# Kernel tuning notes

Measured on AMD Instinct MI355X. Metric: run time of the kernel, lower is better.

The kernel has to match this reference:

```python
import jax, jax.numpy as jnp
import numpy as np

NEG_SLOPE = 0.2  # PyG GATConv default leaky_relu slope


def gat_conv(x, src, dst, W, att_src, att_dst, bias, num_nodes):
    """PyG-style GATConv with concat=False (mean over heads).
    x: [N, Fin], src/dst: [E] (self-loops already appended),
    W: [Fin, H*C], att_src/att_dst: [H, C], bias: [C].
    """
    H, C = att_src.shape
    h = (x @ W).reshape(num_nodes, H, C)               # [N, H, C]
    a_s = jnp.sum(h * att_src[None], axis=-1)          # [N, H]
    a_d = jnp.sum(h * att_dst[None], axis=-1)          # [N, H]
    e = jax.nn.leaky_relu(a_s[src] + a_d[dst], NEG_SLOPE)  # [E, H]
    # softmax over incoming edges per destination node
    e_max = jax.ops.segment_max(e, dst, num_segments=num_nodes)  # [N, H]
    e_exp = jnp.exp(e - e_max[dst])
    denom = jax.ops.segment_sum(e_exp, dst, num_segments=num_nodes)
    alpha = e_exp / (denom[dst] + 1e-16)               # [E, H]
    msg = h[src] * alpha[:, :, None]                   # [E, H, C]
    out = jax.ops.segment_sum(msg, dst, num_segments=num_nodes)  # [N, H, C]
    return out.mean(axis=1) + bias                     # concat=False -> head mean


def setup_inputs() -> dict:
    N, E = 100000, 1600000
    Fin, Hid, Fout, Hds = 128, 64, 32, 2
    key = jax.random.key(0)
    ks = jax.random.split(key, 12)
    glorot = lambda k, shape, fan: (jax.random.normal(k, shape, jnp.float32) / np.sqrt(fan))
    return {
        "x": jax.random.normal(ks[0], (N, Fin), jnp.float32),
        "edge_index": jax.random.randint(ks[1], (2, E), 0, N, jnp.int64 if jax.config.read("jax_enable_x64") else jnp.int32),
        "W1": glorot(ks[2], (Fin, Hds * Hid), Fin),
        "att_src1": glorot(ks[3], (Hds, Hid), Hid),
        "att_dst1": glorot(ks[4], (Hds, Hid), Hid),
        "b1": jnp.zeros((Hid,), jnp.float32),
        "W2": glorot(ks[5], (Hid, Hds * Fout), Hid),
        "att_src2": glorot(ks[6], (Hds, Fout), Fout),
        "att_dst2": glorot(ks[7], (Hds, Fout), Fout),
        "b2": jnp.zeros((Fout,), jnp.float32),
    }


def reference(x, edge_index, W1, att_src1, att_dst1, b1, W2, att_src2, att_dst2, b2):
    N = x.shape[0]
    # PyG GATConv default: add self-loops
    loops = jnp.arange(N, dtype=edge_index.dtype)
    src = jnp.concatenate([edge_index[0], loops])
    dst = jnp.concatenate([edge_index[1], loops])
    # dropout(p=0.6) is identity in eval mode
    h = gat_conv(x, src, dst, W1, att_src1, att_dst1, b1, N)
    h = jax.nn.elu(h)
    out = gat_conv(h, src, dst, W2, att_src2, att_dst2, b2, N)
    return out
```

## Files before the change

### kernel.cpp

```cpp
#include <hip/hip_runtime.h>
#include <hip/hip_bf16.h>
#include <hip/hip_fp16.h>
#include <math.h>


#define BINBITS 9
#define NBUCK 256
#define CHUNK 4096
#define SPANCAP 12288

typedef _Float16 half8 __attribute__((ext_vector_type(8)));
typedef float f32x4 __attribute__((ext_vector_type(4)));


__global__ void init_kernel(int* __restrict__ bcnt) {
    bcnt[threadIdx.x] = 0;
}

__global__ void bucket_hist_kernel(const int* __restrict__ dst, int* __restrict__ bcnt, int E) {
    __shared__ int h[NBUCK];
    int t = threadIdx.x;
    h[t] = 0;
    __syncthreads();
    for (int i = blockIdx.x * blockDim.x + t; i < E; i += gridDim.x * blockDim.x)
        atomicAdd(&h[dst[i] >> BINBITS], 1);
    __syncthreads();
    if (h[t]) atomicAdd(&bcnt[t], h[t]);
}

__global__ void bucket_scan_kernel(const int* __restrict__ bcnt, int* __restrict__ bbase,
                                   int* __restrict__ bfill) {
    __shared__ int sd[NBUCK];
    int t = threadIdx.x;
    int v = bcnt[t];
    sd[t] = v;
    __syncthreads();
    for (int o = 1; o < NBUCK; o <<= 1) {
        int x = (t >= o) ? sd[t - o] : 0;
        __syncthreads();
        sd[t] += x;
        __syncthreads();
    }
    int exc = sd[t] - v;
    bbase[t] = exc;
    bfill[t] = exc;
    if (t == NBUCK - 1) bbase[NBUCK] = sd[t];
}

__launch_bounds__(256)
__global__ void binA_kernel(const int* __restrict__ esrc, const int* __restrict__ edst,
                            int* __restrict__ bfill, unsigned* __restrict__ binned, int E) {
    __shared__ unsigned stage[CHUNK];
    __shared__ int hcnt[NBUCK], hexc[NBUCK], gb[NBUCK], hfill[NBUCK];
    const int tid = threadIdx.x;
    const int c0 = blockIdx.x * CHUNK;
    const int n = min(CHUNK, E - c0);

    hcnt[tid] = 0;
    hfill[tid] = 0;
    __syncthreads();
    for (int i = tid; i < n; i += 256) atomicAdd(&hcnt[edst[c0 + i] >> BINBITS], 1);
    __syncthreads();
    int myc = hcnt[tid];
    hexc[tid] = myc;
    __syncthreads();
    for (int o = 1; o < NBUCK; o <<= 1) {
        int x = (tid >= o) ? hexc[tid - o] : 0;
        __syncthreads();
        hexc[tid] += x;
        __syncthreads();
    }
    hexc[tid] -= myc;
    gb[tid] = myc ? atomicAdd(&bfill[tid], myc) : 0;
    __syncthreads();

    for (int i = tid; i < n; i += 256) {
        int d = edst[c0 + i], s = esrc[c0 + i];
        int b = d >> BINBITS;
        int p = hexc[b] + atomicAdd(&hfill[b], 1);
        stage[p] = ((unsigned)(d & ((1 << BINBITS) - 1)) << 17) | (unsigned)s;
    }
    __syncthreads();

    const int wid = tid >> 6, lane = tid & 63;
    for (int b = wid * 64; b < wid * 64 + 64; ++b) {
        int cnt = hcnt[b], sb = hexc[b], g = gb[b];
        for (int l = lane; l < cnt; l += 64) binned[g + l] = stage[sb + l];
    }
}

__launch_bounds__(256)
__global__ void binB_kernel(const unsigned* __restrict__ binned, const int* __restrict__ bbase,
                            int* __restrict__ rowptr, int* __restrict__ csr, int N) {
    __shared__ int cnt[512];
    __shared__ int chunk[256];
    __shared__ int excl[513];
    __shared__ int stag[SPANCAP];
    const int tid = threadIdx.x;
    const int b = blockIdx.x;
    const int node0 = b << BINBITS;
    if (node0 >= N) return;
    const int nn = min(512, N - node0);

    cnt[tid] = (tid < nn) ? 1 : 0;
    cnt[tid + 256] = (tid + 256 < nn) ? 1 : 0;
    __syncthreads();
    const int e0 = bbase[b], e1 = bbase[b + 1];
    for (int i = e0 + tid; i < e1; i += 256)
        atomicAdd(&cnt[binned[i] >> 17], 1);
    __syncthreads();

    int c0v = cnt[2 * tid], c1v = cnt[2 * tid + 1];
    chunk[tid] = c0v + c1v;
    __syncthreads();
    int v = chunk[tid];
    for (int o = 1; o < 256; o <<= 1) {
        int x = (tid >= o) ? chunk[tid - o] : 0;
        __syncthreads();
        chunk[tid] += x;
        __syncthreads();
    }
    int cpre = chunk[tid] - v;
    excl[2 * tid] = cpre;
    excl[2 * tid + 1] = cpre + c0v;
    if (tid == 255) excl[512] = cpre + c0v + c1v;
    __syncthreads();

    const int rbase = e0 + node0;
    for (int i = tid; i < nn; i += 256) rowptr[node0 + i] = rbase + excl[i];
    if (node0 + nn >= N && tid == 0) rowptr[N] = rbase + excl[512];

    cnt[tid] = 0;
    cnt[tid + 256] = 0;
    __syncthreads();
    const int span = excl[512];

    if (span <= SPANCAP) {
        for (int i = e0 + tid; i < e1; i += 256) {
            unsigned e = binned[i];
            int dloc = e >> 17, src = e & 0x1FFFF;
            int p = excl[dloc] + atomicAdd(&cnt[dloc], 1);
            stag[p] = src;
        }
        for (int i = tid; i < nn; i += 256) {
            int p = excl[i] + atomicAdd(&cnt[i], 1);
            stag[p] = node0 + i;
        }
        __syncthreads();
        for (int i = tid; i < span; i += 256) csr[rbase + i] = stag[i];
    } else {
        for (int i = e0 + tid; i < e1; i += 256) {
            unsigned e = binned[i];
            int dloc = e >> 17, src = e & 0x1FFFF;
            csr[rbase + excl[dloc] + atomicAdd(&cnt[dloc], 1)] = src;
        }
        for (int i = tid; i < nn; i += 256)
            csr[rbase + excl[i] + atomicAdd(&cnt[i], 1)] = node0 + i;
    }
}


__global__ void wcvt_kernel(const float* __restrict__ W1, _Float16* __restrict__ Wt1,
                            const float* __restrict__ W2, _Float16* __restrict__ Wt2) {
    int i = blockIdx.x * 256 + threadIdx.x;
    if (i < 128 * 128) {
        int n = i >> 7, k = i & 127;
        Wt1[i] = (_Float16)W1[k * 128 + n];
    }
    int j = i - 128 * 128;
    if (j >= 0 && j < 64 * 64) {
        int n = j >> 6, k = j & 63;
        Wt2[j] = (_Float16)W2[k * 64 + n];
    }
}


template <int FIN, int FOUT, typename XT>
__launch_bounds__(256)
__global__ void gemm_attn_mfma(const XT* __restrict__ X, const _Float16* __restrict__ Wt,
                               const float* __restrict__ atts, const float* __restrict__ attd,
                               __half* __restrict__ Hh, float* __restrict__ a_s,
                               float* __restrict__ a_d, int N) {
    constexpr int BM = 128;
    constexpr int C = FOUT / 2;
    constexpr int NT = FOUT / 16;
    constexpr int KS = FIN / 32;
    constexpr int HT = C / 16;
    __shared__ _Float16 sA[BM * FIN];
    __shared__ _Float16 sB[FOUT * FIN];

    const int tid = threadIdx.x;
    const int wv = tid >> 6, ln = tid & 63;
    const int lm = ln & 15, quad = ln >> 4;
    const int row0 = blockIdx.x * BM;

    if (sizeof(XT) == 4) {
        for (int idx = tid; idx < BM * FIN / 4; idx += 256) {
            int r = idx / (FIN / 4), c4 = idx % (FIN / 4);
            int gr = row0 + r;
            float4 v = make_float4(0.f, 0.f, 0.f, 0.f);
            if (gr < N) v = *(const float4*)&((const float*)X)[(size_t)gr * FIN + c4 * 4];
            _Float16 h4[4] = {(_Float16)v.x, (_Float16)v.y, (_Float16)v.z, (_Float16)v.w};
            *(float2*)&sA[r * FIN + c4 * 4] = *(float2*)h4;
        }
    } else {
        for (int idx = tid; idx < BM * FIN / 8; idx += 256) {
            int r = idx / (FIN / 8), c8 = idx % (FIN / 8);
            int gr = row0 + r;
            int4 v = make_int4(0, 0, 0, 0);
            if (gr < N) v = *(const int4*)&((const __half*)X)[(size_t)gr * FIN + c8 * 8];
            *(int4*)&sA[r * FIN + c8 * 8] = v;
        }
    }
    for (int idx = tid; idx < FOUT * FIN / 8; idx += 256)
        *(int4*)&sB[idx * 8] = *(const int4*)&Wt[idx * 8];
    __syncthreads();

    f32x4 acc[2][NT];
#pragma unroll
    for (int mt = 0; mt < 2; ++mt)
#pragma unroll
        for (int nt = 0; nt < NT; ++nt) acc[mt][nt] = f32x4{0.f, 0.f, 0.f, 0.f};

    const int r0 = wv * 32 + lm;
#pragma unroll
    for (int ks = 0; ks < KS; ++ks) {
        int k0 = ks * 32 + quad * 8;
        half8 a0 = *(const half8*)&sA[r0 * FIN + k0];
        half8 a1 = *(const half8*)&sA[(r0 + 16) * FIN + k0];
#pragma unroll
        for (int nt = 0; nt < NT; ++nt) {
            half8 b = *(const half8*)&sB[(nt * 16 + lm) * FIN + k0];
            acc[0][nt] = __builtin_amdgcn_mfma_f32_16x16x32_f16(a0, b, acc[0][nt], 0, 0, 0);
            acc[1][nt] = __builtin_amdgcn_mfma_f32_16x16x32_f16(a1, b, acc[1][nt], 0, 0, 0);
        }
    }

    float psum[2][4][2], pdum[2][4][2];
#pragma unroll
    for (int mt = 0; mt < 2; ++mt)
#pragma unroll
        for (int r = 0; r < 4; ++r) {
            psum[mt][r][0] = psum[mt][r][1] = 0.f;
            pdum[mt][r][0] = pdum[mt][r][1] = 0.f;
        }
#pragma unroll
    for (int nt = 0; nt < NT; ++nt) {
        float av = atts[nt * 16 + lm];
        float dv = attd[nt * 16 + lm];
        int hh = nt / HT;
#pragma unroll
        for (int mt = 0; mt < 2; ++mt)
#pragma unroll
            for (int r = 0; r < 4; ++r) {
                psum[mt][r][hh] = fmaf(acc[mt][nt][r], av, psum[mt][r][hh]);
                pdum[mt][r][hh] = fmaf(acc[mt][nt][r], dv, pdum[mt][r][hh]);
            }
    }
#pragma unroll
    for (int o = 1; o < 16; o <<= 1) {
#pragma unroll
        for (int mt = 0; mt < 2; ++mt)
#pragma unroll
            for (int r = 0; r < 4; ++r) {
                psum[mt][r][0] += __shfl_xor(psum[mt][r][0], o);
                psum[mt][r][1] += __shfl_xor(psum[mt][r][1], o);
                pdum[mt][r][0] += __shfl_xor(pdum[mt][r][0], o);
                pdum[mt][r][1] += __shfl_xor(pdum[mt][r][1], o);
            }
    }
    if (lm == 0) {
#pragma unroll
        for (int mt = 0; mt < 2; ++mt)
#pragma unroll
            for (int r = 0; r < 4; ++r) {
                int gr = row0 + wv * 32 + mt * 16 + quad * 4 + r;
                if (gr < N) {
                    *(float2*)&a_s[gr * 2] = make_float2(psum[mt][r][0], psum[mt][r][1]);
                    *(float2*)&a_d[gr * 2] = make_float2(pdum[mt][r][0], pdum[mt][r][1]);
                }
            }
    }

    __syncthreads();
    _Float16* sH = sA;
#pragma unroll
    for (int mt = 0; mt < 2; ++mt)
#pragma unroll
        for (int nt = 0; nt < NT; ++nt)
#pragma unroll
            for (int r = 0; r < 4; ++r)
                sH[(wv * 32 + mt * 16 + quad * 4 + r) * FOUT + nt * 16 + lm] =
                    (_Float16)acc[mt][nt][r];
    __syncthreads();
    for (int idx = tid; idx < BM * FOUT / 8; idx += 256) {
        int r = idx / (FOUT / 8), c8 = idx % (FOUT / 8);
        int gr = row0 + r;
        if (gr < N)
            *(int4*)&Hh[(size_t)gr * FOUT + c8 * 8] = *(const int4*)&sH[r * FOUT + c8 * 8];
    }
}


__device__ __forceinline__ float lrelu02(float x) { return x > 0.f ? x : 0.2f * x; }

__launch_bounds__(256)
__global__ void edge_w_kernel(const float* __restrict__ a_s, const float* __restrict__ a_d,
                              const int* __restrict__ rowptr, const int* __restrict__ csr,
                              float2* __restrict__ w, int N) {
    const int wid = threadIdx.x >> 6, lane = threadIdx.x & 63;
    int n = blockIdx.x * 4 + wid;
    if (n >= N) return;
    int start = rowptr[n], end = rowptr[n + 1];
    int deg = end - start;
    float2 adn = ((const float2*)a_d)[n];

    if (deg <= 64) {
        float e0 = 0.f, e1 = 0.f;
        int j = start + lane;
        if (lane < deg) {
            int s = csr[j];
            float2 asv = ((const float2*)a_s)[s];
            e0 = __expf(lrelu02(asv.x + adn.x));
            e1 = __expf(lrelu02(asv.y + adn.y));
        }
        float d0 = e0, d1 = e1;
#pragma unroll
        for (int o = 32; o > 0; o >>= 1) {
            d0 += __shfl_xor(d0, o);
            d1 += __shfl_xor(d1, o);
        }
        float i0 = 0.5f / d0, i1 = 0.5f / d1;
        if (lane < deg) w[j] = make_float2(e0 * i0, e1 * i1);
    } else {
        float d0 = 0.f, d1 = 0.f;
        for (int j = start + lane; j < end; j += 64) {
            int s = csr[j];
            float2 asv = ((const float2*)a_s)[s];
            float e0 = __expf(lrelu02(asv.x + adn.x));
            float e1 = __expf(lrelu02(asv.y + adn.y));
            d0 += e0;
            d1 += e1;
            w[j] = make_float2(e0, e1);
        }
#pragma unroll
        for (int o = 32; o > 0; o >>= 1) {
            d0 += __shfl_xor(d0, o);
            d1 += __shfl_xor(d1, o);
        }
        float i0 = 0.5f / d0, i1 = 0.5f / d1;
        for (int j = start + lane; j < end; j += 64) {
            float2 f = w[j];
            w[j] = make_float2(f.x * i0, f.y * i1);
        }
    }
}


template <int C, bool ELU, typename OT>
__launch_bounds__(256)
__global__ void aggregate_kernel(const __half* __restrict__ Hh, const float2* __restrict__ w,
                                 const int* __restrict__ rowptr, const int* __restrict__ csr,
                                 const float* __restrict__ bias, OT* __restrict__ out, int N) {
    constexpr int LPE = (C == 64) ? 16 : 8;
    constexpr int NG = 64 / LPE;
    constexpr int RI = C / 4;
    __shared__ float2 swH[4][64][2];
    const int wid = threadIdx.x >> 6;
    const int lane = threadIdx.x & 63;
    const int sub = lane & (LPE - 1);
    const int qid = lane / LPE;
    const int myH = (sub >= LPE / 2);
    int n = blockIdx.x * 4 + wid;
    if (n >= N) return;
    int start = rowptr[n], end = rowptr[n + 1];
    const int4* HI = (const int4*)Hh;

    float av[8];
#pragma unroll
    for (int j = 0; j < 8; ++j) av[j] = 0.f;

    for (int cs = start; cs < end; cs += 64) {
        int j = cs + lane;
        float2 wv = make_float2(0.f, 0.f);
        int s = 0;
        if (j < end) {
            s = csr[j];
            wv = w[j];
        }
        float fs = __int_as_float(s);
        swH[wid][lane][0] = make_float2(wv.x, fs);
        swH[wid][lane][1] = make_float2(wv.y, fs);
        int cnt = min(64, end - cs);
        int nbatch = (cnt + NG - 1) / NG;
        for (int b = 0; b < nbatch; b += 4) {
            float2 e[4];
#pragma unroll
            for (int u = 0; u < 4; ++u)
                e[u] = swH[wid][(b + u) * NG + qid][myH];
            int4 hv[4];
#pragma unroll
            for (int u = 0; u < 4; ++u)
                hv[u] = HI[(size_t)__float_as_int(e[u].y) * RI + sub];
#pragma unroll
            for (int u = 0; u < 4; ++u) {
                float ww = e[u].x;
                const __half2* h2 = (const __half2*)&hv[u];
#pragma unroll
                for (int p = 0; p < 4; ++p) {
                    float2 f = __half22float2(h2[p]);
                    av[2 * p] = fmaf(ww, f.x, av[2 * p]);
                    av[2 * p + 1] = fmaf(ww, f.y, av[2 * p + 1]);
                }
            }
        }
    }

#pragma unroll
    for (int o = LPE; o < 64; o <<= 1)
#pragma unroll
        for (int j = 0; j < 8; ++j) av[j] += __shfl_xor(av[j], o);
#pragma unroll
    for (int j = 0; j < 8; ++j) av[j] += __shfl_xor(av[j], LPE / 2);

    if (lane < LPE / 2) {
        float4 b0 = *(const float4*)(bias + sub * 8);
        float4 b1 = *(const float4*)(bias + sub * 8 + 4);
        float o0[8];
        o0[0] = av[0] + b0.x; o0[1] = av[1] + b0.y;
        o0[2] = av[2] + b0.z; o0[3] = av[3] + b0.w;
        o0[4] = av[4] + b1.x; o0[5] = av[5] + b1.y;
        o0[6] = av[6] + b1.z; o0[7] = av[7] + b1.w;
        if (ELU) {
#pragma unroll
            for (int j = 0; j < 8; ++j) o0[j] = o0[j] > 0.f ? o0[j] : expm1f(o0[j]);
        }
        if (sizeof(OT) == 2) {
            union { int4 v; __half2 h2[4]; } u;
#pragma unroll
            for (int p = 0; p < 4; ++p) u.h2[p] = __floats2half2_rn(o0[2 * p], o0[2 * p + 1]);
            *(int4*)((__half*)out + (size_t)n * C + sub * 8) = u.v;
        } else {
            *(float4*)((float*)out + (size_t)n * C + sub * 8) =
                make_float4(o0[0], o0[1], o0[2], o0[3]);
            *(float4*)((float*)out + (size_t)n * C + sub * 8 + 4) =
                make_float4(o0[4], o0[5], o0[6], o0[7]);
        }
    }
}


extern "C" void kernel_launch(void* const* d_in, const int* in_sizes, int n_in,
                              void* d_out, int out_size, void* d_ws, size_t ws_size,
                              hipStream_t stream) {
    const float* x    = (const float*)d_in[0];
    const int*   eidx = (const int*)d_in[1];
    const float* W1   = (const float*)d_in[2];
    const float* as1w = (const float*)d_in[3];
    const float* ad1w = (const float*)d_in[4];
    const float* b1   = (const float*)d_in[5];
    const float* W2   = (const float*)d_in[6];
    const float* as2w = (const float*)d_in[7];
    const float* ad2w = (const float*)d_in[8];
    const float* b2   = (const float*)d_in[9];
    float* out = (float*)d_out;

    const int N = in_sizes[0] / 128;
    const int E = in_sizes[1] / 2;
    const int NBK = (N + (1 << BINBITS) - 1) >> BINBITS;

    char* base = (char*)d_ws;
    size_t off = 0;
    auto alloc = [&](size_t bytes) {
        size_t cur = off;
        off += (bytes + 255) & ~(size_t)255;
        return (void*)(base + cur);
    };

    int* rowptr   = (int*)alloc((size_t)(N + 1) * 4);
    int* csr      = (int*)alloc((size_t)(E + N) * 4);
    int* bcnt     = (int*)alloc((size_t)NBUCK * 4);
    int* bbase    = (int*)alloc((size_t)(NBUCK + 1) * 4);
    int* bfill    = (int*)alloc((size_t)NBUCK * 4);
    unsigned* binned = (unsigned*)alloc((size_t)E * 4);
    __half* h1    = (__half*)alloc((size_t)N * 128 * 2);
    __half* x2h   = (__half*)alloc((size_t)N * 64 * 2);
    float* a_s    = (float*)alloc((size_t)N * 2 * 4);
    float* a_d    = (float*)alloc((size_t)N * 2 * 4);
    float2* wEdge = (float2*)alloc((size_t)(E + N) * 8);
    _Float16* Wt1 = (_Float16*)alloc((size_t)128 * 128 * 2);
    _Float16* Wt2 = (_Float16*)alloc((size_t)64 * 64 * 2);

    const int* esrc = eidx;
    const int* edst = eidx + E;

    init_kernel<<<1, NBUCK, 0, stream>>>(bcnt);
    bucket_hist_kernel<<<256, 256, 0, stream>>>(edst, bcnt, E);
    bucket_scan_kernel<<<1, NBUCK, 0, stream>>>(bcnt, bbase, bfill);
    binA_kernel<<<(E + CHUNK - 1) / CHUNK, 256, 0, stream>>>(esrc, edst, bfill, binned, E);
    binB_kernel<<<NBK, 256, 0, stream>>>(binned, bbase, rowptr, csr, N);

    wcvt_kernel<<<(128 * 128 + 64 * 64 + 255) / 256, 256, 0, stream>>>(W1, Wt1, W2, Wt2);

    gemm_attn_mfma<128, 128, float>
        <<<(N + 127) / 128, 256, 0, stream>>>(x, Wt1, as1w, ad1w, h1, a_s, a_d, N);
    edge_w_kernel<<<(N + 3) / 4, 256, 0, stream>>>(a_s, a_d, rowptr, csr, wEdge, N);
    aggregate_kernel<64, true, __half>
        <<<(N + 3) / 4, 256, 0, stream>>>(h1, wEdge, rowptr, csr, b1, x2h, N);

    gemm_attn_mfma<64, 64, __half>
        <<<(N + 127) / 128, 256, 0, stream>>>(x2h, Wt2, as2w, ad2w, h1, a_s, a_d, N);
    edge_w_kernel<<<(N + 3) / 4, 256, 0, stream>>>(a_s, a_d, rowptr, csr, wEdge, N);
    aggregate_kernel<32, false, float>
        <<<(N + 3) / 4, 256, 0, stream>>>(h1, wEdge, rowptr, csr, b2, out, N);
}
```

Baseline: 376.1 us.

## Fuse edge softmax weights into aggregation kernel with deferred normalization

Removes the separate edge_w_kernel and computes unnormalized exp attention scores inside the aggregation kernel, accumulating the softmax denominator alongside the weighted feature sum and scaling once at the end. This eliminates writing and rereading the per-edge float2 weight array (about 13 MB per layer) and two kernel launches. The source index is premultiplied by the row stride, and a scalar tail loop replaces padded batches of four. As before, no max-subtraction is done, so exp overflow stays possible for large logits.

```diff
diff --git a/kernel.cpp b/kernel.cpp
--- a/kernel.cpp
+++ b/kernel.cpp
@@ -304,62 +304,10 @@
 
 __device__ __forceinline__ float lrelu02(float x) { return x > 0.f ? x : 0.2f * x; }
 
-__launch_bounds__(256)
-__global__ void edge_w_kernel(const float* __restrict__ a_s, const float* __restrict__ a_d,
-                              const int* __restrict__ rowptr, const int* __restrict__ csr,
-                              float2* __restrict__ w, int N) {
-    const int wid = threadIdx.x >> 6, lane = threadIdx.x & 63;
-    int n = blockIdx.x * 4 + wid;
-    if (n >= N) return;
-    int start = rowptr[n], end = rowptr[n + 1];
-    int deg = end - start;
-    float2 adn = ((const float2*)a_d)[n];
-
-    if (deg <= 64) {
-        float e0 = 0.f, e1 = 0.f;
-        int j = start + lane;
-        if (lane < deg) {
-            int s = csr[j];
-            float2 asv = ((const float2*)a_s)[s];
-            e0 = __expf(lrelu02(asv.x + adn.x));
-            e1 = __expf(lrelu02(asv.y + adn.y));
-        }
-        float d0 = e0, d1 = e1;
-#pragma unroll
-        for (int o = 32; o > 0; o >>= 1) {
-            d0 += __shfl_xor(d0, o);
-            d1 += __shfl_xor(d1, o);
-        }
-        float i0 = 0.5f / d0, i1 = 0.5f / d1;
-        if (lane < deg) w[j] = make_float2(e0 * i0, e1 * i1);
-    } else {
-        float d0 = 0.f, d1 = 0.f;
-        for (int j = start + lane; j < end; j += 64) {
-            int s = csr[j];
-            float2 asv = ((const float2*)a_s)[s];
-            float e0 = __expf(lrelu02(asv.x + adn.x));
-            float e1 = __expf(lrelu02(asv.y + adn.y));
-            d0 += e0;
-            d1 += e1;
-            w[j] = make_float2(e0, e1);
-        }
-#pragma unroll
-        for (int o = 32; o > 0; o >>= 1) {
-            d0 += __shfl_xor(d0, o);
-            d1 += __shfl_xor(d1, o);
-        }
-        float i0 = 0.5f / d0, i1 = 0.5f / d1;
-        for (int j = start + lane; j < end; j += 64) {
-            float2 f = w[j];
-            w[j] = make_float2(f.x * i0, f.y * i1);
-        }
-    }
-}
-
-
 template <int C, bool ELU, typename OT>
 __launch_bounds__(256)
-__global__ void aggregate_kernel(const __half* __restrict__ Hh, const float2* __restrict__ w,
+__global__ void aggregate_kernel(const __half* __restrict__ Hh,
+                                 const float* __restrict__ a_s, const float* __restrict__ a_d,
                                  const int* __restrict__ rowptr, const int* __restrict__ csr,
                                  const float* __restrict__ bias, OT* __restrict__ out, int N) {
     constexpr int LPE = (C == 64) ? 16 : 8;
@@ -375,25 +323,33 @@
     if (n >= N) return;
     int start = rowptr[n], end = rowptr[n + 1];
     const int4* HI = (const int4*)Hh;
+    float2 adn = ((const float2*)a_d)[n];
 
     float av[8];
 #pragma unroll
     for (int j = 0; j < 8; ++j) av[j] = 0.f;
+    float d0 = 0.f, d1 = 0.f;
 
     for (int cs = start; cs < end; cs += 64) {
         int j = cs + lane;
-        float2 wv = make_float2(0.f, 0.f);
-        int s = 0;
+        float e0 = 0.f, e1 = 0.f;
+        int sri = 0;
         if (j < end) {
-            s = csr[j];
-            wv = w[j];
-        }
-        float fs = __int_as_float(s);
-        swH[wid][lane][0] = make_float2(wv.x, fs);
-        swH[wid][lane][1] = make_float2(wv.y, fs);
+            int s = csr[j];
+            sri = s * RI;
+            float2 asv = ((const float2*)a_s)[s];
+            e0 = __expf(lrelu02(asv.x + adn.x));
+            e1 = __expf(lrelu02(asv.y + adn.y));
+        }
+        d0 += e0;
+        d1 += e1;
+        float fs = __int_as_float(sri);
+        swH[wid][lane][0] = make_float2(e0, fs);
+        swH[wid][lane][1] = make_float2(e1, fs);
         int cnt = min(64, end - cs);
         int nbatch = (cnt + NG - 1) / NG;
-        for (int b = 0; b < nbatch; b += 4) {
+        int b = 0;
+        for (; b + 4 <= nbatch; b += 4) {
             float2 e[4];
 #pragma unroll
             for (int u = 0; u < 4; ++u)
@@ -401,7 +357,7 @@
             int4 hv[4];
 #pragma unroll
             for (int u = 0; u < 4; ++u)
-                hv[u] = HI[(size_t)__float_as_int(e[u].y) * RI + sub];
+                hv[u] = HI[(size_t)(__float_as_int(e[u].y) + sub)];
 #pragma unroll
             for (int u = 0; u < 4; ++u) {
                 float ww = e[u].x;
@@ -414,12 +370,32 @@
                 }
             }
         }
+        for (; b < nbatch; ++b) {
+            float2 ev = swH[wid][b * NG + qid][myH];
+            int4 hv = HI[(size_t)(__float_as_int(ev.y) + sub)];
+            float ww = ev.x;
+            const __half2* h2 = (const __half2*)&hv;
+#pragma unroll
+            for (int p = 0; p < 4; ++p) {
+                float2 f = __half22float2(h2[p]);
+                av[2 * p] = fmaf(ww, f.x, av[2 * p]);
+                av[2 * p + 1] = fmaf(ww, f.y, av[2 * p + 1]);
+            }
+        }
     }
 
 #pragma unroll
     for (int o = LPE; o < 64; o <<= 1)
 #pragma unroll
         for (int j = 0; j < 8; ++j) av[j] += __shfl_xor(av[j], o);
+#pragma unroll
+    for (int o = 32; o > 0; o >>= 1) {
+        d0 += __shfl_xor(d0, o);
+        d1 += __shfl_xor(d1, o);
+    }
+    float sc = myH ? (0.5f / d1) : (0.5f / d0);
+#pragma unroll
+    for (int j = 0; j < 8; ++j) av[j] *= sc;
 #pragma unroll
     for (int j = 0; j < 8; ++j) av[j] += __shfl_xor(av[j], LPE / 2);
 
@@ -487,7 +463,6 @@
     __half* x2h   = (__half*)alloc((size_t)N * 64 * 2);
     float* a_s    = (float*)alloc((size_t)N * 2 * 4);
     float* a_d    = (float*)alloc((size_t)N * 2 * 4);
-    float2* wEdge = (float2*)alloc((size_t)(E + N) * 8);
     _Float16* Wt1 = (_Float16*)alloc((size_t)128 * 128 * 2);
     _Float16* Wt2 = (_Float16*)alloc((size_t)64 * 64 * 2);
 
@@ -504,13 +479,11 @@
 
     gemm_attn_mfma<128, 128, float>
         <<<(N + 127) / 128, 256, 0, stream>>>(x, Wt1, as1w, ad1w, h1, a_s, a_d, N);
-    edge_w_kernel<<<(N + 3) / 4, 256, 0, stream>>>(a_s, a_d, rowptr, csr, wEdge, N);
     aggregate_kernel<64, true, __half>
-        <<<(N + 3) / 4, 256, 0, stream>>>(h1, wEdge, rowptr, csr, b1, x2h, N);
+        <<<(N + 3) / 4, 256, 0, stream>>>(h1, a_s, a_d, rowptr, csr, b1, x2h, N);
 
     gemm_attn_mfma<64, 64, __half>
         <<<(N + 127) / 128, 256, 0, stream>>>(x2h, Wt2, as2w, ad2w, h1, a_s, a_d, N);
-    edge_w_kernel<<<(N + 3) / 4, 256, 0, stream>>>(a_s, a_d, rowptr, csr, wEdge, N);
     aggregate_kernel<32, false, float>
-        <<<(N + 3) / 4, 256, 0, stream>>>(h1, wEdge, rowptr, csr, b2, out, N);
-}
+        <<<(N + 3) / 4, 256, 0, stream>>>(h1, a_s, a_d, rowptr, csr, b2, out, N);
+}
```

Result: faster. 353.7 us (-5.9%).
